# Optimization experiments

Measured on AMD Instinct MI355X. Metric: run time of the kernel, lower is better.

## Reference

```python
import jax, jax.numpy as jnp
import numpy as np

N_NODES = 100000
N_EDGES = 1600000
D_IN = 64
D_OUT = 64


def setup_inputs() -> dict:
    key = jax.random.key(0)
    k1, k2, k3, k4 = jax.random.split(key, 4)
    feat = jax.random.normal(k1, (N_NODES, D_IN), dtype=jnp.float32)
    edge_src = jax.random.randint(k2, (N_EDGES,), 0, N_NODES, dtype=jnp.int64)
    edge_dst = jax.random.randint(k3, (N_EDGES,), 0, N_NODES, dtype=jnp.int64)
    # xavier_uniform with gain for relu (sqrt(2)) on [out, in] Linear weight
    gain = float(np.sqrt(2.0))
    limit = gain * float(np.sqrt(6.0 / (D_IN + D_OUT)))
    fc_weight = jax.random.uniform(k4, (D_OUT, D_IN), dtype=jnp.float32,
                                   minval=-limit, maxval=limit)
    return {"feat": feat, "edge_src": edge_src, "edge_dst": edge_dst,
            "fc_weight": fc_weight}


def reference(feat, edge_src, edge_dst, fc_weight):
    # SDDMM: edge score a_e = <h_src, h_dst>  (fn.u_dot_v)
    h_src = feat[edge_src]                      # [E, d]
    h_dst = feat[edge_dst]                      # [E, d]
    a = jnp.sum(h_src * h_dst, axis=-1, keepdims=True)  # [E, 1]
    # SpMM: neigh[v] = sum_{(u->v)} h_u * a_e  (u_mul_e + sum)
    m = h_src * a                               # [E, d]
    neigh = jax.ops.segment_sum(m, edge_dst, num_segments=feat.shape[0])  # [N, d]
    # Linear without bias: y = neigh @ W.T
    return neigh @ fc_weight.T
```

## Files before the change

### kernel.cpp

```cpp
#include <hip/hip_runtime.h>

#define N_NODES 100000
#define N_EDGES 1600000
#define D 64
#define NB 782
#define CAP 3072
#define EPB 8192
#define NPART ((N_EDGES + EPB - 1) / EPB)
#define RSH 14

typedef unsigned short ushort_t;
typedef unsigned int uint_t;

__device__ __forceinline__ ushort_t f2bf(float f) {
    uint_t u = __float_as_uint(f);
    u += 0x7FFF + ((u >> 16) & 1);
    return (ushort_t)(u >> 16);
}

__global__ __launch_bounds__(256) void repack_init(const float* __restrict__ feat,
                                                   ushort_t* __restrict__ featb,
                                                   int* __restrict__ gcur) {
    const int tid = blockIdx.x * 256 + threadIdx.x;
    if (tid < NB) gcur[tid] = tid * CAP;
    const int base = tid * 16;
    if (base >= N_NODES * D) return;
    const float4* f4 = (const float4*)(feat + base);
    ushort4* o4 = (ushort4*)(featb + base);
#pragma unroll
    for (int j = 0; j < 4; ++j) {
        const float4 v = f4[j];
        o4[j] = make_ushort4(f2bf(v.x), f2bf(v.y), f2bf(v.z), f2bf(v.w));
    }
}

__global__ __launch_bounds__(1024) void partition(const int* __restrict__ esrc,
                                                  const int* __restrict__ edst,
                                                  int* __restrict__ gcur,
                                                  int* __restrict__ slab) {
    __shared__ int stage[EPB];
    __shared__ ushort_t bkt16[EPB];
    __shared__ int cnt[NB];
    __shared__ int cur[NB];
    __shared__ int gb[NB];
    __shared__ int s[1024];
    const int t = threadIdx.x;
    const int base = blockIdx.x * EPB;
    const int n = min(EPB, N_EDGES - base);

    if (t < NB) cnt[t] = 0;
    __syncthreads();
    for (int i = t; i < n; i += 1024)
        atomicAdd(&cnt[edst[base + i] >> 7], 1);
    __syncthreads();
    const int v = (t < NB) ? cnt[t] : 0;
    s[t] = v;
    __syncthreads();
    for (int off = 1; off < 1024; off <<= 1) {
        const int x = (t >= off) ? s[t - off] : 0;
        __syncthreads();
        s[t] += x;
        __syncthreads();
    }
    if (t < NB) {
        const int excl = s[t] - v;
        cur[t] = excl;
        gb[t] = (v ? atomicAdd(&gcur[t], v) : 0) - excl;
    }
    __syncthreads();
    for (int i = t; i < n; i += 1024) {
        const int d = edst[base + i];
        const int bkt = d >> 7;
        const int pos = atomicAdd(&cur[bkt], 1);
        stage[pos] = ((d & 127) << 17) | esrc[base + i];
        bkt16[pos] = (ushort_t)bkt;
    }
    __syncthreads();
    for (int i = t; i < n; i += 1024) {
        const int bkt = bkt16[i];
        const int gp = gb[bkt] + i;
        if (gp < (bkt + 1) * CAP)
            slab[gp] = stage[i];
    }
}

template<int CTRL>
__device__ __forceinline__ float fadd_dpp(float x) {
    const int r = __builtin_amdgcn_update_dpp(0, __float_as_int(x), CTRL, 0xF, 0xF, true);
    return x + __int_as_float(r);
}
__device__ __forceinline__ float red8(float p) {
    p = fadd_dpp<0xB1>(p);
    p = fadd_dpp<0x4E>(p);
    p = fadd_dpp<0x141>(p);
    return p;
}

__device__ __forceinline__ float cvt_dot(const uint4 u, const float* __restrict__ h,
                                         float* __restrict__ g) {
    g[0] = __uint_as_float(u.x << 16); g[1] = __uint_as_float(u.x & 0xFFFF0000u);
    g[2] = __uint_as_float(u.y << 16); g[3] = __uint_as_float(u.y & 0xFFFF0000u);
    g[4] = __uint_as_float(u.z << 16); g[5] = __uint_as_float(u.z & 0xFFFF0000u);
    g[6] = __uint_as_float(u.w << 16); g[7] = __uint_as_float(u.w & 0xFFFF0000u);
    float p = 0.f;
#pragma unroll
    for (int k = 0; k < 8; ++k) p += g[k] * h[k];
    return p;
}

#define SMEM_BYTES 51200
#define OFF_SEB    12288
#define OFF_CNT    24576
#define OFF_CUR    28672
#define OFF_S      32768
#define OFF_ROW    34816
#define OFF_DEG    35332
#define OFF_PERM   35844
#define OFF_WT     33792

#define EDGE_ROUND(ACC, LN)                                                    \
    if ((LN) < nb_nodes) {                                                     \
        float h[8];                                                            \
        {                                                                      \
            const int nidx = nbase + (LN);                                     \
            const float4 ha = feat4[nidx * 16 + 2 * l];                        \
            const float4 hb = feat4[nidx * 16 + 2 * l + 1];                    \
            h[0] = ha.x; h[1] = ha.y; h[2] = ha.z; h[3] = ha.w;                \
            h[4] = hb.x; h[5] = hb.y; h[6] = hb.z; h[7] = hb.w;                \
        }                                                                      \
        int e = rowoff[(LN)];                                                  \
        const int e1 = rowoff[(LN) + 1];                                       \
        for (; e + 3 < e1; e += 4) {                                           \
            const int s0 = seB[e], s1 = seB[e + 1];                            \
            const int s2 = seB[e + 2], s3 = seB[e + 3];                        \
            const uint4 u0 = featb4[s0 * 8 + l];                               \
            const uint4 u1 = featb4[s1 * 8 + l];                               \
            const uint4 u2 = featb4[s2 * 8 + l];                               \
            const uint4 u3 = featb4[s3 * 8 + l];                               \
            float g0[8], g1[8], g2[8], g3[8];                                  \
            float p0 = cvt_dot(u0, h, g0);                                     \
            float p1 = cvt_dot(u1, h, g1);                                     \
            float p2 = cvt_dot(u2, h, g2);                                     \
            float p3 = cvt_dot(u3, h, g3);                                     \
            p0 = red8(p0); p1 = red8(p1); p2 = red8(p2); p3 = red8(p3);        \
            _Pragma("unroll")                                                  \
            for (int k = 0; k < 8; ++k)                                        \
                ACC[k] += g0[k] * p0 + g1[k] * p1 + g2[k] * p2 + g3[k] * p3;   \
        }                                                                      \
        for (; e < e1; ++e) {                                                  \
            const uint4 u0 = featb4[seB[e] * 8 + l];                           \
            float g0[8];                                                       \
            float p0 = red8(cvt_dot(u0, h, g0));                               \
            _Pragma("unroll")                                                  \
            for (int k = 0; k < 8; ++k) ACC[k] += g0[k] * p0;                  \
        }                                                                      \
    }

__global__ __launch_bounds__(512, 6) void fused_spmm_gemm(
        const float4* __restrict__ feat4,
        const uint4* __restrict__ featb4,
        const int* __restrict__ slab,
        const int* __restrict__ gcur,
        const float* __restrict__ W,
        float4* __restrict__ out4) {
    __shared__ __align__(16) char smem[SMEM_BYTES];
    int* seA    = (int*)(smem);
    int* seB    = (int*)(smem + OFF_SEB);
    int* cnt    = (int*)(smem + OFF_CNT);
    int* cur    = (int*)(smem + OFF_CUR);
    int* s      = (int*)(smem + OFF_S);
    int* rowoff = (int*)(smem + OFF_ROW);
    int* degs   = (int*)(smem + OFF_DEG);
    int* perm   = (int*)(smem + OFF_PERM);
    float (*nT)[132] = (float(*)[132])(smem);
    float (*WT)[68]  = (float(*)[68])(smem + OFF_WT);

    const int t = threadIdx.x;
    const int b = blockIdx.x;
    const int nbase = b << 7;
    const int nb_nodes = min(128, N_NODES - nbase);
    const int sbase = b * CAP;
    const int ne = min(gcur[b] - sbase, CAP);

    for (int i = t; i < ne; i += 512) seA[i] = slab[sbase + i];
    cnt[t] = 0; cnt[t + 512] = 0;
    __syncthreads();
    for (int i = t; i < ne; i += 512) {
        const int pk = seA[i];
        atomicAdd(&cnt[((pk >> 17) << 3) | ((pk & 0x1FFFF) >> RSH)], 1);
    }
    __syncthreads();
    const int v0 = cnt[2 * t], v1 = cnt[2 * t + 1];
    const int sum = v0 + v1;
    s[t] = sum;
    __syncthreads();
    for (int off = 1; off < 512; off <<= 1) {
        const int x = (t >= off) ? s[t - off] : 0;
        __syncthreads();
        s[t] += x;
        __syncthreads();
    }
    const int excl = s[t] - sum;
    cur[2 * t] = excl;
    cur[2 * t + 1] = excl + v0;
    __syncthreads();
    if (t < 128) rowoff[t] = cur[t << 3];
    if (t == 0) rowoff[128] = ne;
    __syncthreads();
    if (t < 128) degs[t] = rowoff[t + 1] - rowoff[t];
    for (int i = t; i < ne; i += 512) {
        const int pk = seA[i];
        const int key = ((pk >> 17) << 3) | ((pk & 0x1FFFF) >> RSH);
        const int pos = atomicAdd(&cur[key], 1);
        seB[pos] = pk & 0x1FFFF;
    }
    __syncthreads();
    if (t < 128) {
        const int d = degs[t];
        int pos = 0;
        for (int j = 0; j < 128; ++j) {
            const int dj = degs[j];
            pos += (dj < d) || (dj == d && j < t);
        }
        perm[pos] = t;
    }
    __syncthreads();

    const int slot = t >> 3;
    const int l = t & 7;
    const int ln0 = perm[slot];
    const int ln1 = perm[127 - slot];
    float acc0[8], acc1[8];
#pragma unroll
    for (int k = 0; k < 8; ++k) { acc0[k] = 0.f; acc1[k] = 0.f; }
    EDGE_ROUND(acc0, ln0)
    EDGE_ROUND(acc1, ln1)
    __syncthreads();

#pragma unroll
    for (int k = 0; k < 8; ++k) nT[8 * l + k][ln0] = acc0[k];
#pragma unroll
    for (int k = 0; k < 8; ++k) nT[8 * l + k][ln1] = acc1[k];
    {
        const float4* W4 = (const float4*)W;
#pragma unroll
        for (int j = 0; j < 2; ++j) {
            const int f = t + j * 512;
            const int o = f >> 4;
            const int i4 = (f & 15) * 4;
            const float4 w = W4[f];
            WT[i4 + 0][o] = w.x;
            WT[i4 + 1][o] = w.y;
            WT[i4 + 2][o] = w.z;
            WT[i4 + 3][o] = w.w;
        }
    }
    __syncthreads();

    const int c4 = (t & 15) * 4;
    const int r0 = (t >> 4) * 4;
    float a4[4][4];
#pragma unroll
    for (int r = 0; r < 4; ++r)
#pragma unroll
        for (int c = 0; c < 4; ++c) a4[r][c] = 0.f;

    for (int i = 0; i < 64; ++i) {
        const float4 w = *(const float4*)&WT[i][c4];
        const float4 rv = *(const float4*)&nT[i][r0];
        const float wv[4] = {w.x, w.y, w.z, w.w};
        const float rr[4] = {rv.x, rv.y, rv.z, rv.w};
#pragma unroll
        for (int r = 0; r < 4; ++r)
#pragma unroll
            for (int c = 0; c < 4; ++c) a4[r][c] += rr[r] * wv[c];
    }

#pragma unroll
    for (int r = 0; r < 4; ++r) {
        const int rr = r0 + r;
        if (rr < nb_nodes)
            out4[(long)(nbase + rr) * 16 + (t & 15)] =
                make_float4(a4[r][0], a4[r][1], a4[r][2], a4[r][3]);
    }
}

extern "C" void kernel_launch(void* const* d_in, const int* in_sizes, int n_in,
                              void* d_out, int out_size, void* d_ws, size_t ws_size,
                              hipStream_t stream) {
    const float* feat = (const float*)d_in[0];
    const int*   esrc = (const int*)d_in[1];
    const int*   edst = (const int*)d_in[2];
    const float* W    = (const float*)d_in[3];
    float* out = (float*)d_out;

    char* ws = (char*)d_ws;
    ushort_t* featb = (ushort_t*)(ws);
    int* slab = (int*)(ws + 12800000);
    int* gcur = (int*)(ws + 12800000 + (size_t)NB * CAP * 4);

    repack_init<<<(N_NODES * D / 16 + 255) / 256, 256, 0, stream>>>(feat, featb, gcur);
    partition<<<NPART, 1024, 0, stream>>>(esrc, edst, gcur, slab);
    fused_spmm_gemm<<<NB, 512, 0, stream>>>((const float4*)feat, (const uint4*)featb,
                                            slab, gcur, W, (float4*)out);
}
```

Measured before the change: 191.5 us.

## Cut LDS footprint, drop degree sort, split GEMM into two halves

```diff
diff --git a/kernel.cpp b/kernel.cpp
--- a/kernel.cpp
+++ b/kernel.cpp
@@ -108,15 +108,13 @@
     return p;
 }
 
-#define SMEM_BYTES 51200
-#define OFF_SEB    12288
+#define SMEM_BYTES 35840
+#define OFF_SEA    12288
 #define OFF_CNT    24576
 #define OFF_CUR    28672
 #define OFF_S      32768
 #define OFF_ROW    34816
-#define OFF_DEG    35332
-#define OFF_PERM   35844
-#define OFF_WT     33792
+#define OFF_HN     12288
 
 #define EDGE_ROUND(ACC, LN)                                                    \
     if ((LN) < nb_nodes) {                                                     \
@@ -156,7 +154,38 @@
         }                                                                      \
     }
 
-__global__ __launch_bounds__(512, 6) void fused_spmm_gemm(
+#define GEMM_HALF(HBASE)                                                       \
+    {                                                                          \
+        const int r0 = (t >> 4) * 2;                                           \
+        const int c4 = (t & 15) * 4;                                           \
+        float a00 = 0.f, a01 = 0.f, a02 = 0.f, a03 = 0.f;                      \
+        float a10 = 0.f, a11 = 0.f, a12 = 0.f, a13 = 0.f;                      \
+        for (int i4 = 0; i4 < 16; ++i4) {                                      \
+            const float4 x0 = *(const float4*)&hN[r0][i4 * 4];                 \
+            const float4 x1 = *(const float4*)&hN[r0 + 1][i4 * 4];             \
+            const float4 w0 = W4[(c4 + 0) * 16 + i4];                          \
+            const float4 w1 = W4[(c4 + 1) * 16 + i4];                          \
+            const float4 w2 = W4[(c4 + 2) * 16 + i4];                          \
+            const float4 w3 = W4[(c4 + 3) * 16 + i4];                          \
+            a00 += x0.x * w0.x + x0.y * w0.y + x0.z * w0.z + x0.w * w0.w;      \
+            a01 += x0.x * w1.x + x0.y * w1.y + x0.z * w1.z + x0.w * w1.w;      \
+            a02 += x0.x * w2.x + x0.y * w2.y + x0.z * w2.z + x0.w * w2.w;      \
+            a03 += x0.x * w3.x + x0.y * w3.y + x0.z * w3.z + x0.w * w3.w;      \
+            a10 += x1.x * w0.x + x1.y * w0.y + x1.z * w0.z + x1.w * w0.w;      \
+            a11 += x1.x * w1.x + x1.y * w1.y + x1.z * w1.z + x1.w * w1.w;      \
+            a12 += x1.x * w2.x + x1.y * w2.y + x1.z * w2.z + x1.w * w2.w;      \
+            a13 += x1.x * w3.x + x1.y * w3.y + x1.z * w3.z + x1.w * w3.w;      \
+        }                                                                      \
+        const int row = (HBASE) + r0;                                          \
+        if (row < nb_nodes)                                                    \
+            out4[(long)(nbase + row) * 16 + (t & 15)] =                        \
+                make_float4(a00, a01, a02, a03);                               \
+        if (row + 1 < nb_nodes)                                                \
+            out4[(long)(nbase + row + 1) * 16 + (t & 15)] =                    \
+                make_float4(a10, a11, a12, a13);                               \
+    }
+
+__global__ __launch_bounds__(512) void fused_spmm_gemm(
         const float4* __restrict__ feat4,
         const uint4* __restrict__ featb4,
         const int* __restrict__ slab,
@@ -164,16 +193,13 @@
         const float* __restrict__ W,
         float4* __restrict__ out4) {
     __shared__ __align__(16) char smem[SMEM_BYTES];
-    int* seA    = (int*)(smem);
-    int* seB    = (int*)(smem + OFF_SEB);
+    int* seB    = (int*)(smem);
+    int* seA    = (int*)(smem + OFF_SEA);
     int* cnt    = (int*)(smem + OFF_CNT);
     int* cur    = (int*)(smem + OFF_CUR);
     int* s      = (int*)(smem + OFF_S);
     int* rowoff = (int*)(smem + OFF_ROW);
-    int* degs   = (int*)(smem + OFF_DEG);
-    int* perm   = (int*)(smem + OFF_PERM);
-    float (*nT)[132] = (float(*)[132])(smem);
-    float (*WT)[68]  = (float(*)[68])(smem + OFF_WT);
+    float (*hN)[68] = (float(*)[68])(smem + OFF_HN);
 
     const int t = threadIdx.x;
     const int b = blockIdx.x;
@@ -181,6 +207,7 @@
     const int nb_nodes = min(128, N_NODES - nbase);
     const int sbase = b * CAP;
     const int ne = min(gcur[b] - sbase, CAP);
+    const float4* W4 = (const float4*)W;
 
     for (int i = t; i < ne; i += 512) seA[i] = slab[sbase + i];
     cnt[t] = 0; cnt[t + 512] = 0;
@@ -207,7 +234,6 @@
     if (t < 128) rowoff[t] = cur[t << 3];
     if (t == 0) rowoff[128] = ne;
     __syncthreads();
-    if (t < 128) degs[t] = rowoff[t + 1] - rowoff[t];
     for (int i = t; i < ne; i += 512) {
         const int pk = seA[i];
         const int key = ((pk >> 17) << 3) | ((pk & 0x1FFFF) >> RSH);
@@ -215,74 +241,26 @@
         seB[pos] = pk & 0x1FFFF;
     }
     __syncthreads();
-    if (t < 128) {
-        const int d = degs[t];
-        int pos = 0;
-        for (int j = 0; j < 128; ++j) {
-            const int dj = degs[j];
-            pos += (dj < d) || (dj == d && j < t);
-        }
-        perm[pos] = t;
-    }
-    __syncthreads();
 
     const int slot = t >> 3;
     const int l = t & 7;
-    const int ln0 = perm[slot];
-    const int ln1 = perm[127 - slot];
     float acc0[8], acc1[8];
 #pragma unroll
     for (int k = 0; k < 8; ++k) { acc0[k] = 0.f; acc1[k] = 0.f; }
-    EDGE_ROUND(acc0, ln0)
-    EDGE_ROUND(acc1, ln1)
-    __syncthreads();
-
-#pragma unroll
-    for (int k = 0; k < 8; ++k) nT[8 * l + k][ln0] = acc0[k];
-#pragma unroll
-    for (int k = 0; k < 8; ++k) nT[8 * l + k][ln1] = acc1[k];
-    {
-        const float4* W4 = (const float4*)W;
-#pragma unroll
-        for (int j = 0; j < 2; ++j) {
-            const int f = t + j * 512;
-            const int o = f >> 4;
-            const int i4 = (f & 15) * 4;
-            const float4 w = W4[f];
-            WT[i4 + 0][o] = w.x;
-            WT[i4 + 1][o] = w.y;
-            WT[i4 + 2][o] = w.z;
-            WT[i4 + 3][o] = w.w;
-        }
-    }
-    __syncthreads();
-
-    const int c4 = (t & 15) * 4;
-    const int r0 = (t >> 4) * 4;
-    float a4[4][4];
-#pragma unroll
-    for (int r = 0; r < 4; ++r)
-#pragma unroll
-        for (int c = 0; c < 4; ++c) a4[r][c] = 0.f;
-
-    for (int i = 0; i < 64; ++i) {
-        const float4 w = *(const float4*)&WT[i][c4];
-        const float4 rv = *(const float4*)&nT[i][r0];
-        const float wv[4] = {w.x, w.y, w.z, w.w};
-        const float rr[4] = {rv.x, rv.y, rv.z, rv.w};
-#pragma unroll
-        for (int r = 0; r < 4; ++r)
-#pragma unroll
-            for (int c = 0; c < 4; ++c) a4[r][c] += rr[r] * wv[c];
-    }
-
-#pragma unroll
-    for (int r = 0; r < 4; ++r) {
-        const int rr = r0 + r;
-        if (rr < nb_nodes)
-            out4[(long)(nbase + rr) * 16 + (t & 15)] =
-                make_float4(a4[r][0], a4[r][1], a4[r][2], a4[r][3]);
-    }
+
+    EDGE_ROUND(acc0, slot)
+    *(float4*)&hN[slot][8 * l]     = make_float4(acc0[0], acc0[1], acc0[2], acc0[3]);
+    *(float4*)&hN[slot][8 * l + 4] = make_float4(acc0[4], acc0[5], acc0[6], acc0[7]);
+
+    EDGE_ROUND(acc1, slot + 64)
+
+    __syncthreads();
+    GEMM_HALF(0)
+    __syncthreads();
+    *(float4*)&hN[slot][8 * l]     = make_float4(acc1[0], acc1[1], acc1[2], acc1[3]);
+    *(float4*)&hN[slot][8 * l + 4] = make_float4(acc1[4], acc1[5], acc1[6], acc1[7]);
+    __syncthreads();
+    GEMM_HALF(64)
 }
 
 extern "C" void kernel_launch(void* const* d_in, const int* in_sizes, int n_in,
```

Result: slower. 558.1 us (+191.5%).
